# Kernel optimization log

Measured on AMD Instinct MI355X. Metric: run time of the kernel, lower is better.

## Reference

```python
import jax, jax.numpy as jnp
import numpy as np


def conv2d_reflect(x, w, b, stride):
    # 3x3 conv, padding=1, padding_mode='reflect'
    x = jnp.pad(x, ((0, 0), (0, 0), (1, 1), (1, 1)), mode='reflect')
    y = jax.lax.conv_general_dilated(x, w, (stride, stride), 'VALID',
                                     dimension_numbers=('NCHW', 'OIHW', 'NCHW'))
    return y + b[None, :, None, None]


def avg_pool(x, k):
    B, C, H, W = x.shape
    return x.reshape(B, C, H // k, k, W // k, k).mean(axis=(3, 5))


def _interp_axis(x, size_out, axis):
    # 1D linear interpolation with align_corners=True semantics
    size_in = x.shape[axis]
    pos = jnp.linspace(0.0, size_in - 1.0, size_out)
    i0 = jnp.clip(jnp.floor(pos).astype(jnp.int32), 0, size_in - 2)
    frac = (pos - i0.astype(x.dtype))
    shape = [1] * x.ndim
    shape[axis] = size_out
    frac = frac.reshape(shape)
    a = jnp.take(x, i0, axis=axis)
    b = jnp.take(x, i0 + 1, axis=axis)
    return a + frac * (b - a)


def resize_bilinear_ac(x, oh, ow):
    return _interp_axis(_interp_axis(x, oh, 2), ow, 3)


def _forward(img, conv1_w, conv1_b, conv2_w, conv2_b, conv3_w, conv3_b,
             conv4_w, conv4_b, lin1_w, lin1_b, lin2_w, lin2_b, luts):
    B, C, H, W = img.shape
    silu = jax.nn.silu
    # --- feature branch on fixed 256x256 resize ---
    x = resize_bilinear_ac(img, 256, 256)
    c1 = silu(conv2d_reflect(x, conv1_w, conv1_b, 2))    # [B,32,128,128]
    c2 = silu(conv2d_reflect(c1, conv2_w, conv2_b, 2))   # [B,64,64,64]
    c3 = silu(conv2d_reflect(c2, conv3_w, conv3_b, 2))   # [B,128,32,32]
    c4 = silu(conv2d_reflect(c3, conv4_w, conv4_b, 2))   # [B,256,16,16]
    feat = jnp.concatenate([avg_pool(c1, 16), avg_pool(c2, 8),
                            avg_pool(c3, 4), avg_pool(c4, 2)], axis=1)  # [B,480,8,8]
    h1 = silu(conv2d_reflect(feat, lin1_w, lin1_b, 1))   # [B,128,8,8]
    wl = jax.lax.conv_general_dilated(h1, lin2_w, (1, 1), 'VALID',
                                      dimension_numbers=('NCHW', 'OIHW', 'NCHW'))
    wl = jax.nn.sigmoid(wl + lin2_b[None, :, None, None])  # [B,27,8,8]
    weights = resize_bilinear_ac(wl, H, W)               # [B, C*K, H, W]
    # --- adaptive 1D LUT transform (per-pixel interpolated gather) ---
    Cl, K, N = luts.shape
    pos = jnp.clip(img, 0.0, 1.0) * (N - 1)
    i0 = jnp.clip(jnp.floor(pos).astype(jnp.int32), 0, N - 2)  # [B,C,H,W]
    frac = pos - i0.astype(pos.dtype)
    cidx = jnp.arange(Cl)[None, :, None, None, None]
    kidx = jnp.arange(K)[None, None, :, None, None]
    iexp = i0[:, :, None, :, :]
    v0 = luts[cidx, kidx, iexp]          # [B,C,K,H,W]
    v1 = luts[cidx, kidx, iexp + 1]
    val = v0 + frac[:, :, None, :, :] * (v1 - v0)
    wts = weights.reshape(B, Cl, K, H, W)
    return jnp.einsum('bckhw,bckhw->bchw', wts, val)


def setup_inputs() -> dict:
    key = jax.random.key(0)
    ks = jax.random.split(key, 10)
    s = 0.05
    return {
        'img': jax.random.uniform(ks[0], (2, 3, 1024, 1024), dtype=jnp.float32),
        'conv1_w': jax.random.normal(ks[1], (32, 3, 3, 3), dtype=jnp.float32) * s,
        'conv1_b': jnp.zeros((32,), jnp.float32),
        'conv2_w': jax.random.normal(ks[2], (64, 32, 3, 3), dtype=jnp.float32) * s,
        'conv2_b': jnp.zeros((64,), jnp.float32),
        'conv3_w': jax.random.normal(ks[3], (128, 64, 3, 3), dtype=jnp.float32) * s,
        'conv3_b': jnp.zeros((128,), jnp.float32),
        'conv4_w': jax.random.normal(ks[4], (256, 128, 3, 3), dtype=jnp.float32) * s,
        'conv4_b': jnp.zeros((256,), jnp.float32),
        'lin1_w': jax.random.normal(ks[5], (128, 480, 3, 3), dtype=jnp.float32) * s,
        'lin1_b': jnp.zeros((128,), jnp.float32),
        'lin2_w': jax.random.normal(ks[6], (27, 128, 1, 1), dtype=jnp.float32) * s,
        'lin2_b': jnp.zeros((27,), jnp.float32),
        'luts': jax.random.normal(ks[7], (3, 9, 256), dtype=jnp.float32),
    }


def reference(img, conv1_w, conv1_b, conv2_w, conv2_b, conv3_w, conv3_b,
              conv4_w, conv4_b, lin1_w, lin1_b, lin2_w, lin2_b, luts):
    out = _forward(img, conv1_w, conv1_b, conv2_w, conv2_b, conv3_w, conv3_b,
                   conv4_w, conv4_b, lin1_w, lin1_b, lin2_w, lin2_b, luts)
    return jnp.clip(out, 0.0, 1.0)
```

## Files before the change

kernel.cpp:

```cpp
#include <hip/hip_runtime.h>

#define DI __device__ __forceinline__

DI float silu_f(float x) { return x / (1.f + __expf(-x)); }
DI float sigmoid_f(float x) { return 1.f / (1.f + __expf(-x)); }
DI int reflect_i(int i, int n) { if (i < 0) i = -i; if (i >= n) i = 2 * n - 2 - i; return i; }

__global__ __launch_bounds__(256) void k_resize(const float* __restrict__ img,
                                                float* __restrict__ x) {
    __shared__ float r0s[1024], r1s[1024];
    const int oy = blockIdx.x & 255;
    const int bc = blockIdx.x >> 8;
    float py = oy * (1023.f / 255.f);
    int iy0 = (int)py; if (iy0 > 1022) iy0 = 1022;
    float fy = py - (float)iy0;
    const float* p0 = img + ((size_t)bc * 1024 + iy0) * 1024;
    ((float4*)r0s)[threadIdx.x] = ((const float4*)p0)[threadIdx.x];
    ((float4*)r1s)[threadIdx.x] = ((const float4*)(p0 + 1024))[threadIdx.x];
    __syncthreads();
    const int ox = threadIdx.x;
    float px = ox * (1023.f / 255.f);
    int ix0 = (int)px; if (ix0 > 1022) ix0 = 1022;
    float fx = px - (float)ix0;
    float a00 = r0s[ix0], a01 = r0s[ix0 + 1];
    float a10 = r1s[ix0], a11 = r1s[ix0 + 1];
    float r0v = a00 + fy * (a10 - a00);
    float r1v = a01 + fy * (a11 - a01);
    x[((size_t)bc * 256 + oy) * 256 + ox] = r0v + fx * (r1v - r0v);
}

template<int CIN, int HIN, int WIN, int COUT>
__global__ __launch_bounds__(256) void k_conv_woc(const float* __restrict__ in,
                                                  const float* __restrict__ w,
                                                  const float* __restrict__ bias,
                                                  float* __restrict__ out) {
    constexpr int HOUT = HIN / 2, WOUT = WIN / 2;
    constexpr int NPXU = 2 * HOUT * WOUT;
    constexpr int NB_PX = NPXU / 64;

    __shared__ float sw[8 * CIN * 12];
    const int tid = threadIdx.x;
    const int ocu = blockIdx.x / NB_PX;
    const int bpx = blockIdx.x % NB_PX;
    {
        const float* src = w + (size_t)(ocu * 8) * CIN * 9;
        for (int i = tid; i < 8 * CIN * 9; i += 256)
            sw[(i / 9) * 12 + (i % 9)] = src[i];
    }
    __syncthreads();

    const int wave = tid >> 6, lane = tid & 63;
    const int pxu = bpx * 64 + lane;
    const int ox = pxu % WOUT;
    const int oy = (pxu / WOUT) % HOUT;
    const int bb = pxu / (WOUT * HOUT);

    int iy[3], xs[3];
#pragma unroll
    for (int k = 0; k < 3; ++k) {
        iy[k] = reflect_i(2 * oy + k - 1, HIN);
        xs[k] = reflect_i(2 * ox + k - 1, WIN);
    }

    float acc[2] = {0.f, 0.f};
    for (int ic = 0; ic < CIN; ++ic) {
        const float* ib = in + ((size_t)bb * CIN + ic) * HIN * WIN;
        float t[3][3];
#pragma unroll
        for (int ky = 0; ky < 3; ++ky) {
            const float* rp = ib + iy[ky] * WIN;
#pragma unroll
            for (int kx = 0; kx < 3; ++kx) t[ky][kx] = rp[xs[kx]];
        }
#pragma unroll
        for (int o = 0; o < 2; ++o) {
            const float* wp = sw + ((size_t)(wave * 2 + o) * CIN + ic) * 12;
            float wv[9];
#pragma unroll
            for (int j = 0; j < 9; ++j) wv[j] = wp[j];
#pragma unroll
            for (int ky = 0; ky < 3; ++ky)
#pragma unroll
                for (int kx = 0; kx < 3; ++kx)
                    acc[o] = fmaf(t[ky][kx], wv[ky * 3 + kx], acc[o]);
        }
    }

#pragma unroll
    for (int o = 0; o < 2; ++o) {
        const int oc = ocu * 8 + wave * 2 + o;
        out[(((size_t)bb * COUT + oc) * HOUT + oy) * WOUT + ox] =
            silu_f(acc[o] + bias[oc]);
    }
}

template<int CIN, int HIN, int WIN, int COUT, int OC_PER>
__global__ __launch_bounds__(256) void k_conv_w4(const float* __restrict__ in,
                                                 const float* __restrict__ w,
                                                 const float* __restrict__ bias,
                                                 float* __restrict__ out) {
    constexpr int HOUT = HIN / 2, WOUT = WIN / 2;
    constexpr int NPXU = 2 * HOUT * WOUT;
    constexpr int NB_PX = NPXU / 64;
    constexpr int ICC = CIN / 4;

    __shared__ float sw[OC_PER * CIN * 12];
    __shared__ float sred[4][OC_PER][64];
    const int tid = threadIdx.x;
    const int ocu = blockIdx.x / NB_PX;
    const int bpx = blockIdx.x % NB_PX;
    {
        const float* src = w + (size_t)(ocu * OC_PER) * CIN * 9;
        for (int i = tid; i < OC_PER * CIN * 9; i += 256)
            sw[(i / 9) * 12 + (i % 9)] = src[i];
    }
    __syncthreads();

    const int kc = tid >> 6;
    const int lane = tid & 63;
    const int pxu = bpx * 64 + lane;
    const int ox = pxu % WOUT;
    const int oy = (pxu / WOUT) % HOUT;
    const int bb = pxu / (WOUT * HOUT);

    int iy[3], xs[3];
#pragma unroll
    for (int k = 0; k < 3; ++k) {
        iy[k] = reflect_i(2 * oy + k - 1, HIN);
        xs[k] = reflect_i(2 * ox + k - 1, WIN);
    }

    float acc[OC_PER];
#pragma unroll
    for (int o = 0; o < OC_PER; ++o) acc[o] = 0.f;

    for (int icl = 0; icl < ICC; ++icl) {
        const int ic = kc * ICC + icl;
        const float* ib = in + ((size_t)bb * CIN + ic) * HIN * WIN;
        float t[3][3];
#pragma unroll
        for (int ky = 0; ky < 3; ++ky) {
            const float* rp = ib + iy[ky] * WIN;
#pragma unroll
            for (int kx = 0; kx < 3; ++kx) t[ky][kx] = rp[xs[kx]];
        }
#pragma unroll
        for (int o = 0; o < OC_PER; ++o) {
            const float* wp = sw + ((size_t)o * CIN + ic) * 12;
            float wv[9];
#pragma unroll
            for (int j = 0; j < 9; ++j) wv[j] = wp[j];
#pragma unroll
            for (int ky = 0; ky < 3; ++ky)
#pragma unroll
                for (int kx = 0; kx < 3; ++kx)
                    acc[o] = fmaf(t[ky][kx], wv[ky * 3 + kx], acc[o]);
        }
    }

#pragma unroll
    for (int o = 0; o < OC_PER; ++o) sred[kc][o][lane] = acc[o];
    __syncthreads();
    if (kc < OC_PER) {
        const int o = kc;
        const int oc = ocu * OC_PER + o;
        float s = sred[0][o][lane] + sred[1][o][lane] + sred[2][o][lane] + sred[3][o][lane];
        out[(((size_t)bb * COUT + oc) * HOUT + oy) * WOUT + ox] = silu_f(s + bias[oc]);
    }
}

__global__ void k_pool(const float* __restrict__ c1, const float* __restrict__ c2,
                       const float* __restrict__ c3, const float* __restrict__ c4,
                       float* __restrict__ feat) {
    int idx = blockIdx.x * blockDim.x + threadIdx.x;
    if (idx >= 2 * 480 * 64) return;
    int x = idx & 7;
    int y = (idx >> 3) & 7;
    int fc = (idx >> 6) % 480;
    int bb = idx / (480 * 64);
    const float* src; int C, HW, k, c;
    if (fc < 32)       { src = c1; C = 32;  HW = 128; k = 16; c = fc; }
    else if (fc < 96)  { src = c2; C = 64;  HW = 64;  k = 8;  c = fc - 32; }
    else if (fc < 224) { src = c3; C = 128; HW = 32;  k = 4;  c = fc - 96; }
    else               { src = c4; C = 256; HW = 16;  k = 2;  c = fc - 224; }
    const float* p = src + ((size_t)bb * C + c) * HW * HW + (y * k) * HW + x * k;
    float s = 0.f;
    if (k >= 4) {
        for (int i = 0; i < k; ++i) {
            const float4* r4 = (const float4*)(p + i * HW);
            for (int j = 0; j < k / 4; ++j) {
                float4 q = r4[j];
                s += q.x + q.y + q.z + q.w;
            }
        }
    } else {
        for (int i = 0; i < k; ++i)
            for (int j = 0; j < k; ++j) s += p[i * HW + j];
    }
    feat[idx] = s / (float)(k * k);
}

__global__ __launch_bounds__(512) void k_lin1(const float* __restrict__ feat,
                                              const float* __restrict__ w,
                                              const float* __restrict__ bias,
                                              float* __restrict__ h1) {
    __shared__ float sw[480 * 9];
    __shared__ float sred[8][64];
    const int tid = threadIdx.x;
    const int bb = blockIdx.x >> 7;
    const int oc = blockIdx.x & 127;
    {
        const float* src = w + (size_t)oc * 480 * 9;
        for (int i = tid; i < 480 * 9; i += 512) sw[i] = src[i];
    }
    const int wave = tid >> 6;
    const int lane = tid & 63;
    const int py = lane >> 3, px = lane & 7;
    int srcl[9];
#pragma unroll
    for (int ky = 0; ky < 3; ++ky)
#pragma unroll
        for (int kx = 0; kx < 3; ++kx)
            srcl[ky * 3 + kx] = reflect_i(py + ky - 1, 8) * 8 + reflect_i(px + kx - 1, 8);
    __syncthreads();

    const float* fp = feat + (size_t)bb * 480 * 64;
    float acc = 0.f;
    for (int ic = wave * 60; ic < wave * 60 + 60; ++ic) {
        float v = fp[ic * 64 + lane];
        const float* wp = sw + ic * 9;
#pragma unroll
        for (int j = 0; j < 9; ++j)
            acc = fmaf(__shfl(v, srcl[j], 64), wp[j], acc);
    }
    sred[wave][lane] = acc;
    __syncthreads();
    if (wave == 0) {
        float s = 0.f;
#pragma unroll
        for (int wv = 0; wv < 8; ++wv) s += sred[wv][lane];
        h1[((size_t)bb * 128 + oc) * 64 + lane] = silu_f(s + bias[oc]);
    }
}

__global__ __launch_bounds__(256) void k_apply(const float* __restrict__ img,
                                               const float* __restrict__ h1,
                                               const float* __restrict__ l2w,
                                               const float* __restrict__ l2b,
                                               const float* __restrict__ luts,
                                               float* __restrict__ out) {
    __shared__ float2 slut2[9 * 256];
    __shared__ float swl[9 * 64];
    __shared__ float su8[8 * 72];
    const int tid = threadIdx.x;
    const int bc = blockIdx.y;
    const int bb = bc / 3, c = bc % 3;

    for (int i = tid; i < 9 * 256; i += 256) {
        int k = i >> 8, j = i & 255;
        const float* lp = luts + (size_t)(c * 9 + k) * 256;
        float v0 = lp[j];
        float v1 = lp[j < 255 ? j + 1 : 255];
        slut2[i] = make_float2(v0, v1);
    }
    {
        const float* hp = h1 + (size_t)bb * 128 * 64;
        const int pix = tid & 63;
        for (int o = tid >> 6; o < 9; o += 4) {
            const float* wp = l2w + (size_t)(c * 9 + o) * 128;
            float s = l2b[c * 9 + o];
            for (int ic = 0; ic < 128; ++ic) s = fmaf(hp[ic * 64 + pix], wp[ic], s);
            swl[o * 64 + pix] = sigmoid_f(s);
        }
    }
    __syncthreads();
    for (int i = tid; i < 576; i += 256) {
        int rr = i / 72, rem = i % 72;
        int k = rem >> 3, xx = rem & 7;
        int h = blockIdx.x * 8 + rr;
        float py = h * (7.f / 1023.f);
        int iy0 = (int)py; if (iy0 > 6) iy0 = 6;
        float fy = py - (float)iy0;
        float a = swl[k * 64 + iy0 * 8 + xx];
        float b = swl[k * 64 + iy0 * 8 + 8 + xx];
        su8[i] = fmaf(fy, b - a, a);
    }
    __syncthreads();

    const int x0 = tid * 4;
    float fx[4]; int sel[4]; int cbase;
    {
        float p0 = x0 * (7.f / 1023.f);
        int ib = (int)p0; if (ib > 6) ib = 6;
        cbase = ib;
#pragma unroll
        for (int p = 0; p < 4; ++p) {
            float pxf = (x0 + p) * (7.f / 1023.f);
            int i = (int)pxf; if (i > 6) i = 6;
            sel[p] = i - cbase;
            fx[p] = pxf - (float)i;
        }
    }
    const size_t plane = ((size_t)bb * 3 + c) * 1024;

    for (int rr = 0; rr < 8; ++rr) {
        const int h = blockIdx.x * 8 + rr;
        const size_t base = (plane + h) * 1024;
        float4 v = ((const float4*)(img + base))[tid];
        float xin[4] = {v.x, v.y, v.z, v.w};
        int i0[4]; float fr[4]; float acc[4] = {0.f, 0.f, 0.f, 0.f};
#pragma unroll
        for (int p = 0; p < 4; ++p) {
            float pv = fminf(fmaxf(xin[p], 0.f), 1.f) * 255.f;
            int i = (int)pv; if (i > 254) i = 254;
            i0[p] = i; fr[p] = pv - (float)i;
        }
        const float* srow = su8 + rr * 72;
#pragma unroll
        for (int k = 0; k < 9; ++k) {
            float s0 = srow[k * 8 + cbase];
            float s1 = srow[k * 8 + cbase + 1];
            float s2 = (cbase < 6) ? srow[k * 8 + cbase + 2] : s1;
            const float2* lrow = slut2 + k * 256;
#pragma unroll
            for (int p = 0; p < 4; ++p) {
                float a = sel[p] ? s1 : s0;
                float b = sel[p] ? s2 : s1;
                float wt = fmaf(fx[p], b - a, a);
                float2 l = lrow[i0[p]];
                acc[p] = fmaf(wt, fmaf(fr[p], l.y - l.x, l.x), acc[p]);
            }
        }
        float4 o4 = make_float4(fminf(fmaxf(acc[0], 0.f), 1.f),
                                fminf(fmaxf(acc[1], 0.f), 1.f),
                                fminf(fmaxf(acc[2], 0.f), 1.f),
                                fminf(fmaxf(acc[3], 0.f), 1.f));
        ((float4*)(out + base))[tid] = o4;
    }
}

extern "C" void kernel_launch(void* const* d_in, const int* in_sizes, int n_in,
                              void* d_out, int out_size, void* d_ws, size_t ws_size,
                              hipStream_t stream) {
    const float* img     = (const float*)d_in[0];
    const float* conv1_w = (const float*)d_in[1];
    const float* conv1_b = (const float*)d_in[2];
    const float* conv2_w = (const float*)d_in[3];
    const float* conv2_b = (const float*)d_in[4];
    const float* conv3_w = (const float*)d_in[5];
    const float* conv3_b = (const float*)d_in[6];
    const float* conv4_w = (const float*)d_in[7];
    const float* conv4_b = (const float*)d_in[8];
    const float* lin1_w  = (const float*)d_in[9];
    const float* lin1_b  = (const float*)d_in[10];
    const float* lin2_w  = (const float*)d_in[11];
    const float* lin2_b  = (const float*)d_in[12];
    const float* luts    = (const float*)d_in[13];
    float* out = (float*)d_out;

    float* ws = (float*)d_ws;
    float* x_rs = ws;            ws += 2 * 3 * 256 * 256;
    float* c1   = ws;            ws += 2 * 32 * 128 * 128;
    float* c2   = ws;            ws += 2 * 64 * 64 * 64;
    float* c3   = ws;            ws += 2 * 128 * 32 * 32;
    float* c4   = ws;            ws += 2 * 256 * 16 * 16;
    float* feat = ws;            ws += 2 * 480 * 8 * 8;
    float* h1   = ws;            ws += 2 * 128 * 8 * 8;

    const int B = 256;
    k_resize<<<6 * 256, B, 0, stream>>>(img, x_rs);
    k_conv_woc<3, 256, 256, 32><<<2048, B, 0, stream>>>(x_rs, conv1_w, conv1_b, c1);
    k_conv_woc<32, 128, 128, 64><<<1024, B, 0, stream>>>(c1, conv2_w, conv2_b, c2);
    k_conv_w4<64, 64, 64, 128, 2><<<2048, B, 0, stream>>>(c2, conv3_w, conv3_b, c3);
    k_conv_w4<128, 32, 32, 256, 2><<<1024, B, 0, stream>>>(c3, conv4_w, conv4_b, c4);
    k_pool<<<(2 * 480 * 64 + B - 1) / B, B, 0, stream>>>(c1, c2, c3, c4, feat);
    k_lin1<<<256, 512, 0, stream>>>(feat, lin1_w, lin1_b, h1);
    dim3 agrid(128, 6);
    k_apply<<<agrid, B, 0, stream>>>(img, h1, lin2_w, lin2_b, luts, out);
}
```

Before: 249.2 us.

## Split lin2 into own kernel, rework pooling, widen conv grids, halve apply rows

Moves the 1x1 lin2 conv and sigmoid out of the apply kernel into a separate small kernel, so the 128-long dot products are no longer recomputed by every apply block. Rewrites pooling with wave-cooperative coalesced loads and shuffle reductions. Conv2 and conv4 now use one output channel per wave and twice as many blocks. The apply kernel handles 4 rows per block instead of 8, with a 2x larger grid, and prefetches the next image row. Each change aims to raise parallelism and cut redundant work, at the cost of an extra launch and more weight reloads into shared memory.

```diff
diff --git a/kernel.cpp b/kernel.cpp
--- a/kernel.cpp
+++ b/kernel.cpp
@@ -29,22 +29,22 @@
     x[((size_t)bc * 256 + oy) * 256 + ox] = r0v + fx * (r1v - r0v);
 }
 
-template<int CIN, int HIN, int WIN, int COUT>
+template<int CIN, int HIN, int WIN, int COUT, int OCW>
 __global__ __launch_bounds__(256) void k_conv_woc(const float* __restrict__ in,
                                                   const float* __restrict__ w,
                                                   const float* __restrict__ bias,
                                                   float* __restrict__ out) {
     constexpr int HOUT = HIN / 2, WOUT = WIN / 2;
-    constexpr int NPXU = 2 * HOUT * WOUT;
-    constexpr int NB_PX = NPXU / 64;
-
-    __shared__ float sw[8 * CIN * 12];
+    constexpr int NB_PX = 2 * HOUT * WOUT / 64;
+    constexpr int NOC = 4 * OCW;
+
+    __shared__ float sw[NOC * CIN * 12];
     const int tid = threadIdx.x;
     const int ocu = blockIdx.x / NB_PX;
     const int bpx = blockIdx.x % NB_PX;
     {
-        const float* src = w + (size_t)(ocu * 8) * CIN * 9;
-        for (int i = tid; i < 8 * CIN * 9; i += 256)
+        const float* src = w + (size_t)(ocu * NOC) * CIN * 9;
+        for (int i = tid; i < NOC * CIN * 9; i += 256)
             sw[(i / 9) * 12 + (i % 9)] = src[i];
     }
     __syncthreads();
@@ -62,7 +62,10 @@
         xs[k] = reflect_i(2 * ox + k - 1, WIN);
     }
 
-    float acc[2] = {0.f, 0.f};
+    float acc[OCW];
+#pragma unroll
+    for (int o = 0; o < OCW; ++o) acc[o] = 0.f;
+
     for (int ic = 0; ic < CIN; ++ic) {
         const float* ib = in + ((size_t)bb * CIN + ic) * HIN * WIN;
         float t[3][3];
@@ -73,8 +76,8 @@
             for (int kx = 0; kx < 3; ++kx) t[ky][kx] = rp[xs[kx]];
         }
 #pragma unroll
-        for (int o = 0; o < 2; ++o) {
-            const float* wp = sw + ((size_t)(wave * 2 + o) * CIN + ic) * 12;
+        for (int o = 0; o < OCW; ++o) {
+            const float* wp = sw + ((size_t)(wave * OCW + o) * CIN + ic) * 12;
             float wv[9];
 #pragma unroll
             for (int j = 0; j < 9; ++j) wv[j] = wp[j];
@@ -87,8 +90,8 @@
     }
 
 #pragma unroll
-    for (int o = 0; o < 2; ++o) {
-        const int oc = ocu * 8 + wave * 2 + o;
+    for (int o = 0; o < OCW; ++o) {
+        const int oc = ocu * NOC + wave * OCW + o;
         out[(((size_t)bb * COUT + oc) * HOUT + oy) * WOUT + ox] =
             silu_f(acc[o] + bias[oc]);
     }
@@ -100,8 +103,7 @@
                                                  const float* __restrict__ bias,
                                                  float* __restrict__ out) {
     constexpr int HOUT = HIN / 2, WOUT = WIN / 2;
-    constexpr int NPXU = 2 * HOUT * WOUT;
-    constexpr int NB_PX = NPXU / 64;
+    constexpr int NB_PX = 2 * HOUT * WOUT / 64;
     constexpr int ICC = CIN / 4;
 
     __shared__ float sw[OC_PER * CIN * 12];
@@ -169,35 +171,63 @@
     }
 }
 
-__global__ void k_pool(const float* __restrict__ c1, const float* __restrict__ c2,
-                       const float* __restrict__ c3, const float* __restrict__ c4,
-                       float* __restrict__ feat) {
-    int idx = blockIdx.x * blockDim.x + threadIdx.x;
-    if (idx >= 2 * 480 * 64) return;
-    int x = idx & 7;
-    int y = (idx >> 3) & 7;
-    int fc = (idx >> 6) % 480;
-    int bb = idx / (480 * 64);
-    const float* src; int C, HW, k, c;
-    if (fc < 32)       { src = c1; C = 32;  HW = 128; k = 16; c = fc; }
-    else if (fc < 96)  { src = c2; C = 64;  HW = 64;  k = 8;  c = fc - 32; }
-    else if (fc < 224) { src = c3; C = 128; HW = 32;  k = 4;  c = fc - 96; }
-    else               { src = c4; C = 256; HW = 16;  k = 2;  c = fc - 224; }
-    const float* p = src + ((size_t)bb * C + c) * HW * HW + (y * k) * HW + x * k;
-    float s = 0.f;
-    if (k >= 4) {
-        for (int i = 0; i < k; ++i) {
-            const float4* r4 = (const float4*)(p + i * HW);
-            for (int j = 0; j < k / 4; ++j) {
-                float4 q = r4[j];
-                s += q.x + q.y + q.z + q.w;
-            }
-        }
+__global__ __launch_bounds__(256) void k_pool(const float* __restrict__ c1,
+                                              const float* __restrict__ c2,
+                                              const float* __restrict__ c3,
+                                              const float* __restrict__ c4,
+                                              float* __restrict__ feat) {
+    const int tid = threadIdx.x;
+    const int W = blockIdx.x * 4 + (tid >> 6);
+    const int lane = tid & 63;
+    if (W < 512) {
+        int bb = W >> 8, rem = W & 255;
+        int c = rem >> 3, y = rem & 7;
+        const float* p = c1 + ((size_t)bb * 32 + c) * 128 * 128 + (y * 16) * 128 + lane * 2;
+        float s = 0.f;
+#pragma unroll
+        for (int r = 0; r < 16; ++r) {
+            float2 v = *(const float2*)(p + r * 128);
+            s += v.x + v.y;
+        }
+        s += __shfl_xor(s, 1, 64);
+        s += __shfl_xor(s, 2, 64);
+        s += __shfl_xor(s, 4, 64);
+        if ((lane & 7) == 0)
+            feat[((size_t)bb * 480 + c) * 64 + y * 8 + (lane >> 3)] = s * (1.f / 256.f);
+    } else if (W < 1536) {
+        int V = W - 512;
+        int bb = V >> 9, rem = V & 511;
+        int c = rem >> 3, y = rem & 7;
+        const float* p = c2 + ((size_t)bb * 64 + c) * 64 * 64 + (y * 8) * 64 + lane;
+        float s = 0.f;
+#pragma unroll
+        for (int r = 0; r < 8; ++r) s += p[r * 64];
+        s += __shfl_xor(s, 1, 64);
+        s += __shfl_xor(s, 2, 64);
+        s += __shfl_xor(s, 4, 64);
+        if ((lane & 7) == 0)
+            feat[((size_t)bb * 480 + 32 + c) * 64 + y * 8 + (lane >> 3)] = s * (1.f / 64.f);
+    } else if (W < 1792) {
+        int T = (W - 1536) * 64 + lane;
+        int bb = T >> 13, rem = T & 8191;
+        int c = rem >> 6, y = (rem >> 3) & 7, x = rem & 7;
+        const float* p = c3 + ((size_t)bb * 128 + c) * 32 * 32 + (y * 4) * 32 + x * 4;
+        float s = 0.f;
+#pragma unroll
+        for (int r = 0; r < 4; ++r) {
+            float4 v = *(const float4*)(p + r * 32);
+            s += v.x + v.y + v.z + v.w;
+        }
+        feat[((size_t)bb * 480 + 96 + c) * 64 + y * 8 + x] = s * (1.f / 16.f);
     } else {
-        for (int i = 0; i < k; ++i)
-            for (int j = 0; j < k; ++j) s += p[i * HW + j];
-    }
-    feat[idx] = s / (float)(k * k);
+        int T = (W - 1792) * 64 + lane;
+        int bb = T >> 14, rem = T & 16383;
+        int c = rem >> 6, y = (rem >> 3) & 7, x = rem & 7;
+        const float* p = c4 + ((size_t)bb * 256 + c) * 16 * 16 + (y * 2) * 16 + x * 2;
+        float2 v0 = *(const float2*)p;
+        float2 v1 = *(const float2*)(p + 16);
+        feat[((size_t)bb * 480 + 224 + c) * 64 + y * 8 + x] = (v0.x + v0.y + v1.x + v1.y) * 0.25f;
+    }
 }
 
 __global__ __launch_bounds__(512) void k_lin1(const float* __restrict__ feat,
@@ -243,15 +273,27 @@
     }
 }
 
+__global__ void k_lin2(const float* __restrict__ h1, const float* __restrict__ w,
+                       const float* __restrict__ bias, float* __restrict__ wl) {
+    int idx = blockIdx.x * blockDim.x + threadIdx.x;
+    if (idx >= 2 * 27 * 64) return;
+    int pix = idx & 63;
+    int oc = (idx >> 6) % 27;
+    int bb = idx / (27 * 64);
+    const float* hp = h1 + (size_t)bb * 128 * 64 + pix;
+    const float* wp = w + oc * 128;
+    float sum = bias[oc];
+    for (int ic = 0; ic < 128; ++ic) sum = fmaf(hp[ic * 64], wp[ic], sum);
+    wl[((size_t)bb * 27 + oc) * 64 + pix] = sigmoid_f(sum);
+}
+
 __global__ __launch_bounds__(256) void k_apply(const float* __restrict__ img,
-                                               const float* __restrict__ h1,
-                                               const float* __restrict__ l2w,
-                                               const float* __restrict__ l2b,
+                                               const float* __restrict__ wl,
                                                const float* __restrict__ luts,
                                                float* __restrict__ out) {
     __shared__ float2 slut2[9 * 256];
     __shared__ float swl[9 * 64];
-    __shared__ float su8[8 * 72];
+    __shared__ float su4[4 * 72];
     const int tid = threadIdx.x;
     const int bc = blockIdx.y;
     const int bb = bc / 3, c = bc % 3;
@@ -263,27 +305,19 @@
         float v1 = lp[j < 255 ? j + 1 : 255];
         slut2[i] = make_float2(v0, v1);
     }
-    {
-        const float* hp = h1 + (size_t)bb * 128 * 64;
-        const int pix = tid & 63;
-        for (int o = tid >> 6; o < 9; o += 4) {
-            const float* wp = l2w + (size_t)(c * 9 + o) * 128;
-            float s = l2b[c * 9 + o];
-            for (int ic = 0; ic < 128; ++ic) s = fmaf(hp[ic * 64 + pix], wp[ic], s);
-            swl[o * 64 + pix] = sigmoid_f(s);
-        }
-    }
-    __syncthreads();
-    for (int i = tid; i < 576; i += 256) {
+    for (int i = tid; i < 9 * 64; i += 256)
+        swl[i] = wl[((size_t)bb * 27 + c * 9) * 64 + i];
+    __syncthreads();
+    for (int i = tid; i < 288; i += 256) {
         int rr = i / 72, rem = i % 72;
         int k = rem >> 3, xx = rem & 7;
-        int h = blockIdx.x * 8 + rr;
+        int h = blockIdx.x * 4 + rr;
         float py = h * (7.f / 1023.f);
         int iy0 = (int)py; if (iy0 > 6) iy0 = 6;
         float fy = py - (float)iy0;
         float a = swl[k * 64 + iy0 * 8 + xx];
         float b = swl[k * 64 + iy0 * 8 + 8 + xx];
-        su8[i] = fmaf(fy, b - a, a);
+        su4[i] = fmaf(fy, b - a, a);
     }
     __syncthreads();
 
@@ -302,11 +336,12 @@
         }
     }
     const size_t plane = ((size_t)bb * 3 + c) * 1024;
-
-    for (int rr = 0; rr < 8; ++rr) {
-        const int h = blockIdx.x * 8 + rr;
-        const size_t base = (plane + h) * 1024;
-        float4 v = ((const float4*)(img + base))[tid];
+    const int h0 = blockIdx.x * 4;
+
+    float4 v = ((const float4*)(img + (plane + h0) * 1024))[tid];
+    for (int rr = 0; rr < 4; ++rr) {
+        float4 vn = v;
+        if (rr < 3) vn = ((const float4*)(img + (plane + h0 + rr + 1) * 1024))[tid];
         float xin[4] = {v.x, v.y, v.z, v.w};
         int i0[4]; float fr[4]; float acc[4] = {0.f, 0.f, 0.f, 0.f};
 #pragma unroll
@@ -315,7 +350,7 @@
             int i = (int)pv; if (i > 254) i = 254;
             i0[p] = i; fr[p] = pv - (float)i;
         }
-        const float* srow = su8 + rr * 72;
+        const float* srow = su4 + rr * 72;
 #pragma unroll
         for (int k = 0; k < 9; ++k) {
             float s0 = srow[k * 8 + cbase];
@@ -335,7 +370,8 @@
                                 fminf(fmaxf(acc[1], 0.f), 1.f),
                                 fminf(fmaxf(acc[2], 0.f), 1.f),
                                 fminf(fmaxf(acc[3], 0.f), 1.f));
-        ((float4*)(out + base))[tid] = o4;
+        ((float4*)(out + (plane + h0 + rr) * 1024))[tid] = o4;
+        v = vn;
     }
 }
 
@@ -366,15 +402,17 @@
     float* c4   = ws;            ws += 2 * 256 * 16 * 16;
     float* feat = ws;            ws += 2 * 480 * 8 * 8;
     float* h1   = ws;            ws += 2 * 128 * 8 * 8;
+    float* wl   = ws;            ws += 2 * 27 * 8 * 8;
 
     const int B = 256;
     k_resize<<<6 * 256, B, 0, stream>>>(img, x_rs);
-    k_conv_woc<3, 256, 256, 32><<<2048, B, 0, stream>>>(x_rs, conv1_w, conv1_b, c1);
-    k_conv_woc<32, 128, 128, 64><<<1024, B, 0, stream>>>(c1, conv2_w, conv2_b, c2);
+    k_conv_woc<3, 256, 256, 32, 2><<<2048, B, 0, stream>>>(x_rs, conv1_w, conv1_b, c1);
+    k_conv_woc<32, 128, 128, 64, 1><<<2048, B, 0, stream>>>(c1, conv2_w, conv2_b, c2);
     k_conv_w4<64, 64, 64, 128, 2><<<2048, B, 0, stream>>>(c2, conv3_w, conv3_b, c3);
-    k_conv_w4<128, 32, 32, 256, 2><<<1024, B, 0, stream>>>(c3, conv4_w, conv4_b, c4);
-    k_pool<<<(2 * 480 * 64 + B - 1) / B, B, 0, stream>>>(c1, c2, c3, c4, feat);
+    k_conv_w4<128, 32, 32, 256, 1><<<2048, B, 0, stream>>>(c3, conv4_w, conv4_b, c4);
+    k_pool<<<576, B, 0, stream>>>(c1, c2, c3, c4, feat);
     k_lin1<<<256, 512, 0, stream>>>(feat, lin1_w, lin1_b, h1);
-    dim3 agrid(128, 6);
-    k_apply<<<agrid, B, 0, stream>>>(img, h1, lin2_w, lin2_b, luts, out);
-}
+    k_lin2<<<(2 * 27 * 64 + B - 1) / B, B, 0, stream>>>(h1, lin2_w, lin2_b, wl);
+    dim3 agrid(256, 6);
+    k_apply<<<agrid, B, 0, stream>>>(img, wl, luts, out);
+}
```

New measurement: 271.9 us. +9.1%, slower.
